# Optimization experiments

Measured on AMD Instinct MI355X. Metric: run time of the kernel, lower is better.

Reference implementation:

```python
import jax, jax.numpy as jnp
from jax import lax
import numpy as np


def gru_last(seq, Wih, Whh, bih, bhh):
    """Run a torch-style GRU over seq [N, T, C] and return only h_T [N, H].

    Gate order matches torch.nn.GRU: (r, z, n);
    n = tanh(W_in x + b_in + r * (W_hn h + b_hn)).
    """
    N = seq.shape[0]
    H = Whh.shape[1]

    def step(h, x_t):
        gi = x_t @ Wih.T + bih          # [N, 3H]
        gh = h @ Whh.T + bhh            # [N, 3H]
        i_r, i_z, i_n = jnp.split(gi, 3, axis=-1)
        h_r, h_z, h_n = jnp.split(gh, 3, axis=-1)
        r = jax.nn.sigmoid(i_r + h_r)
        z = jax.nn.sigmoid(i_z + h_z)
        n = jnp.tanh(i_n + r * h_n)
        h_new = (1.0 - z) * n + z * h
        return h_new, None

    h0 = jnp.zeros((N, H), dtype=seq.dtype)
    hT, _ = lax.scan(step, h0, jnp.swapaxes(seq, 0, 1))  # scan over T
    return hT


def setup_inputs() -> dict:
    key = jax.random.key(0)
    ks = jax.random.split(key, 12)
    B, C, T, Fq, H = 8, 64, 256, 256, 128
    s = 0.05
    return {
        "x": jax.random.normal(ks[0], (B, C, T, Fq), dtype=jnp.float32),
        "Wih_t": jax.random.normal(ks[1], (3 * H, C), dtype=jnp.float32) * s,
        "Whh_t": jax.random.normal(ks[2], (3 * H, H), dtype=jnp.float32) * s,
        "bih_t": jax.random.normal(ks[3], (3 * H,), dtype=jnp.float32) * s,
        "bhh_t": jax.random.normal(ks[4], (3 * H,), dtype=jnp.float32) * s,
        "Wih_f": jax.random.normal(ks[5], (3 * H, C), dtype=jnp.float32) * s,
        "Whh_f": jax.random.normal(ks[6], (3 * H, H), dtype=jnp.float32) * s,
        "bih_f": jax.random.normal(ks[7], (3 * H,), dtype=jnp.float32) * s,
        "bhh_f": jax.random.normal(ks[8], (3 * H,), dtype=jnp.float32) * s,
        "Wp": jax.random.normal(ks[9], (C, H), dtype=jnp.float32) * s,
        "bp": jax.random.normal(ks[10], (C,), dtype=jnp.float32) * s,
    }


def reference(x, Wih_t, Whh_t, bih_t, bhh_t, Wih_f, Whh_f, bih_f, bhh_f, Wp, bp):
    B, C, T, Fq = x.shape
    H = Whh_t.shape[1]

    # time GRU: sequences of length T, one per (batch, freq)
    t_in = jnp.transpose(x, (0, 3, 2, 1)).reshape(B * Fq, T, C)
    h_t = gru_last(t_in, Wih_t, Whh_t, bih_t, bhh_t)          # [B*F, H]
    t_vec = jnp.transpose(h_t.reshape(B, Fq, H), (0, 2, 1))    # [B, H, F]

    # freq GRU: sequences of length F, one per (batch, time)
    f_in = jnp.transpose(x, (0, 2, 3, 1)).reshape(B * T, Fq, C)
    h_f = gru_last(f_in, Wih_f, Whh_f, bih_f, bhh_f)          # [B*T, H]
    f_vec = jnp.transpose(h_f.reshape(B, T, H), (0, 2, 1))    # [B, H, T]

    # t_feat [B,H,F,1] expanded along dim2 to T (requires F == T),
    # f_feat [B,H,T,1] expanded along dim3 to F; fused is constant along F.
    s = t_vec + f_vec                                          # [B, H, T]  (F == T)
    out_t = jnp.einsum("ch,bht->bct", Wp, s) + bp[None, :, None]  # 1x1 conv
    return jnp.broadcast_to(out_t[:, :, :, None], (B, C, T, Fq))
```

## Files before the change

kernel.cpp:

```cpp
#include <hip/hip_runtime.h>

#define B_ 8
#define C_ 64
#define T_ 256
#define F_ 256
#define H_ 128
#define TF_ (T_*F_)

typedef _Float16 half_t;
typedef _Float16 half8 __attribute__((ext_vector_type(8)));
typedef float float4v __attribute__((ext_vector_type(4)));

#if __has_builtin(__builtin_amdgcn_exp2f)
#define EXP2F(x) __builtin_amdgcn_exp2f(x)
#else
static __device__ inline float EXP2F(float x) { float r; asm("v_exp_f32 %0, %1" : "=v"(r) : "v"(x)); return r; }
#endif
#if __has_builtin(__builtin_amdgcn_rcpf)
#define RCPF(x) __builtin_amdgcn_rcpf(x)
#else
static __device__ inline float RCPF(float x) { float r; asm("v_rcp_f32 %0, %1" : "=v"(r) : "v"(x)); return r; }
#endif

#define NEG_L2E  (-1.4426950408889634f)
#define NEG_2L2E (-2.8853900817779268f)

#define XS_M 72
#define XS_S 1160

__device__ inline half8 load_w8s(const float* __restrict__ p, float s) {
    half8 r;
#pragma unroll
    for (int k = 0; k < 8; ++k) r[k] = (half_t)(p[k] * s);
    return r;
}

#define MFMA(a, b, c) __builtin_amdgcn_mfma_f32_16x16x32_f16((a), (b), (c), 0, 0, 0)

__global__ __launch_bounds__(512, 2) void k_gru(
    const float* __restrict__ x,
    const float* __restrict__ Wih_t, const float* __restrict__ Whh_t,
    const float* __restrict__ bih_t, const float* __restrict__ bhh_t,
    const float* __restrict__ Wih_f, const float* __restrict__ Whh_f,
    const float* __restrict__ bih_f, const float* __restrict__ bhh_f,
    float* __restrict__ h_t_out, float* __restrict__ h_f_out) {
    __shared__ half_t hbuf0[16 * 136];
    __shared__ half_t hbuf1[16 * 136];
    __shared__ half_t xt0[8 * XS_S];
    __shared__ half_t xt1[8 * XS_S];

    int tid  = threadIdx.x;
    int w    = tid >> 6;
    int lane = tid & 63;
    int nidx = lane & 15;
    int quad = lane >> 4;

    int bi  = blockIdx.x;
    bool isf = bi >= 128;
    int lbi = bi & 127;
    int b   = lbi >> 4;
    int g16 = (lbi & 15) << 4;

    const float* Wih = isf ? Wih_f : Wih_t;
    const float* Whh = isf ? Whh_f : Whh_t;
    const float* bih = isf ? bih_f : bih_t;
    const float* bhh = isf ? bhh_f : bhh_t;
    float* hout      = isf ? h_f_out : h_t_out;

    int fq, rowid;
    if (!isf) { fq = tid & 3; rowid = tid >> 2; }
    else      { fq = tid & 1; rowid = tid >> 1; }
    int goff[4], ldsoff[4];
#pragma unroll
    for (int j = 0; j < 4; ++j) {
        int row = rowid + (isf ? 256 : 128) * j;
        int c   = isf ? (row >> 4) : (row >> 3);
        int tl  = isf ? (row & 15) : (row & 7);
        goff[j]   = c * 65536 + tl * 256 + 4 * fq;
        ldsoff[j] = isf ? ((4 * fq) * XS_S + tl * XS_M + c)
                        : (tl * XS_S + (4 * fq) * XS_M + c);
    }
    int estr = isf ? XS_S : XS_M;
    int As8  = isf ? 8 : 8 * 256;
    const float* gb = x + (size_t)b * (64 * 65536) + (size_t)(isf ? g16 * 256 : g16);

#define XLOADG()                                                                \
    {                                                                           \
        _Pragma("unroll")                                                       \
        for (int j = 0; j < 4; ++j) rS[j] = *(const float4v*)(gb + goff[j]);    \
        gb += As8;                                                              \
    }
#define XWRITE(XT)                                                              \
    {                                                                           \
        _Pragma("unroll")                                                       \
        for (int j = 0; j < 4; ++j) {                                           \
            _Pragma("unroll")                                                   \
            for (int e = 0; e < 4; ++e)                                         \
                (XT)[ldsoff[j] + e * estr] = (half_t)rS[j][e];                  \
        }                                                                       \
    }

    int gr = w * 16 + nidx;
    int gz = gr + 128;
    int gn = gr + 256;
    int ko = quad * 8;

    half8 wir0 = load_w8s(Wih + gr * 64 + ko,      NEG_L2E);
    half8 wir1 = load_w8s(Wih + gr * 64 + 32 + ko, NEG_L2E);
    half8 wiz0 = load_w8s(Wih + gz * 64 + ko,      NEG_L2E);
    half8 wiz1 = load_w8s(Wih + gz * 64 + 32 + ko, NEG_L2E);
    half8 win0 = load_w8s(Wih + gn * 64 + ko,      NEG_2L2E);
    half8 win1 = load_w8s(Wih + gn * 64 + 32 + ko, NEG_2L2E);
    half8 whr[4], whz[4], whn[4];
#pragma unroll
    for (int kt = 0; kt < 4; ++kt) {
        whr[kt] = load_w8s(Whh + gr * 128 + kt * 32 + ko, NEG_L2E);
        whz[kt] = load_w8s(Whh + gz * 128 + kt * 32 + ko, NEG_L2E);
        whn[kt] = load_w8s(Whh + gn * 128 + kt * 32 + ko, NEG_2L2E);
    }
    float br  = NEG_L2E  * (bih[gr] + bhh[gr]);
    float bz  = NEG_L2E  * (bih[gz] + bhh[gz]);
    float bin = NEG_2L2E * bih[gn];
    float bhn = NEG_2L2E * bhh[gn];
    float4v brv  = {br, br, br, br};
    float4v bzv  = {bz, bz, bz, bz};
    float4v bnv  = {bin, bin, bin, bin};
    float4v bhnv = {bhn, bhn, bhn, bhn};

    for (int idx = tid; idx < 16 * 136; idx += 512) hbuf0[idx] = (half_t)0.f;
    float h_old[4] = {0.f, 0.f, 0.f, 0.f};

    float4v rS[4];
    XLOADG(); XWRITE(xt0);
    XLOADG(); XWRITE(xt1);
    XLOADG();
    __syncthreads();

    float4v xrE, xzE, xnE;
    {
        const half_t* xrp = xt0 + nidx * XS_M + ko;
        half8 a0 = *(const half8*)xrp;
        half8 a1 = *(const half8*)(xrp + 32);
        xrE = MFMA(a0, wir0, brv); xrE = MFMA(a1, wir1, xrE);
        xzE = MFMA(a0, wiz0, bzv); xzE = MFMA(a1, wiz1, xzE);
        xnE = MFMA(a0, win0, bnv); xnE = MFMA(a1, win1, xnE);
    }
    float4v xrO = {0.f, 0.f, 0.f, 0.f};
    float4v xzO = {0.f, 0.f, 0.f, 0.f};
    float4v xnO = {0.f, 0.f, 0.f, 0.f};

#define GRU_STEP(RBUF, WBUF, XR, XZ, XN, XRn, XZn, XNn, XTB, SROW, REF, STG)    \
    {                                                                           \
        const half_t* hrow = (RBUF) + nidx * 136 + ko;                          \
        half8 ha0 = *(const half8*)(hrow);                                      \
        half8 ha1 = *(const half8*)(hrow + 32);                                 \
        half8 ha2 = *(const half8*)(hrow + 64);                                 \
        half8 ha3 = *(const half8*)(hrow + 96);                                 \
        half8 c0x, c1x;                                                         \
        if (REF) {                                                              \
            const half_t* xrp = (XTB) + (SROW) * XS_S + nidx * XS_M + ko;       \
            c0x = *(const half8*)xrp;                                           \
            c1x = *(const half8*)(xrp + 32);                                    \
        }                                                                       \
        XR = MFMA(ha0, whr[0], XR); XR = MFMA(ha1, whr[1], XR);                 \
        XR = MFMA(ha2, whr[2], XR); XR = MFMA(ha3, whr[3], XR);                 \
        XZ = MFMA(ha0, whz[0], XZ); XZ = MFMA(ha1, whz[1], XZ);                 \
        XZ = MFMA(ha2, whz[2], XZ); XZ = MFMA(ha3, whz[3], XZ);                 \
        float4v hnv = MFMA(ha0, whn[0], bhnv);                                  \
        hnv = MFMA(ha1, whn[1], hnv);                                           \
        float rr[4], Ez[4];                                                     \
        _Pragma("unroll")                                                       \
        for (int rg = 0; rg < 4; ++rg) rr[rg] = RCPF(1.f + EXP2F(XR[rg]));      \
        hnv = MFMA(ha2, whn[2], hnv);                                           \
        hnv = MFMA(ha3, whn[3], hnv);                                           \
        _Pragma("unroll")                                                       \
        for (int rg = 0; rg < 4; ++rg) Ez[rg] = EXP2F(XZ[rg]);                  \
        if (REF) {                                                              \
            XRn = MFMA(c0x, wir0, brv); XRn = MFMA(c1x, wir1, XRn);             \
            XZn = MFMA(c0x, wiz0, bzv); XZn = MFMA(c1x, wiz1, XZn);             \
            XNn = MFMA(c0x, win0, bnv); XNn = MFMA(c1x, win1, XNn);             \
        }                                                                       \
        STG                                                                     \
        _Pragma("unroll")                                                       \
        for (int rg = 0; rg < 4; ++rg) {                                        \
            float np  = XN[rg] + rr[rg] * hnv[rg];                              \
            float En  = EXP2F(np);                                              \
            float u   = __builtin_fmaf(h_old[rg], En, h_old[rg]);               \
            float t2  = u + Ez[rg];                                             \
            float num = __builtin_fmaf(-En, Ez[rg], t2);                        \
            float den = (1.f + En) * (1.f + Ez[rg]);                            \
            float h   = num * RCPF(den);                                        \
            h_old[rg] = h;                                                      \
            (WBUF)[(quad * 4 + rg) * 136 + w * 16 + nidx] = (half_t)h;          \
        }                                                                       \
        __syncthreads();                                                        \
    }

    for (int tt = 0; tt < 16; ++tt) {
        GRU_STEP(hbuf0, hbuf1, xrE, xzE, xnE, xrO, xzO, xnO, xt0, 1, 1, {})
        GRU_STEP(hbuf1, hbuf0, xrO, xzO, xnO, xrE, xzE, xnE, xt0, 2, 1, {})
        GRU_STEP(hbuf0, hbuf1, xrE, xzE, xnE, xrO, xzO, xnO, xt0, 3, 1, {})
        GRU_STEP(hbuf1, hbuf0, xrO, xzO, xnO, xrE, xzE, xnE, xt0, 4, 1, {})
        GRU_STEP(hbuf0, hbuf1, xrE, xzE, xnE, xrO, xzO, xnO, xt0, 5, 1, {})
        GRU_STEP(hbuf1, hbuf0, xrO, xzO, xnO, xrE, xzE, xnE, xt0, 6, 1, {})
        GRU_STEP(hbuf0, hbuf1, xrE, xzE, xnE, xrO, xzO, xnO, xt0, 7, 1, {})
        GRU_STEP(hbuf1, hbuf0, xrO, xzO, xnO, xrE, xzE, xnE, xt1, 0, 1,
                 { if (tt < 15) { XWRITE(xt0); XLOADG(); } })
        GRU_STEP(hbuf0, hbuf1, xrE, xzE, xnE, xrO, xzO, xnO, xt1, 1, 1, {})
        GRU_STEP(hbuf1, hbuf0, xrO, xzO, xnO, xrE, xzE, xnE, xt1, 2, 1, {})
        GRU_STEP(hbuf0, hbuf1, xrE, xzE, xnE, xrO, xzO, xnO, xt1, 3, 1, {})
        GRU_STEP(hbuf1, hbuf0, xrO, xzO, xnO, xrE, xzE, xnE, xt1, 4, 1, {})
        GRU_STEP(hbuf0, hbuf1, xrE, xzE, xnE, xrO, xzO, xnO, xt1, 5, 1, {})
        GRU_STEP(hbuf1, hbuf0, xrO, xzO, xnO, xrE, xzE, xnE, xt1, 6, 1, {})
        GRU_STEP(hbuf0, hbuf1, xrE, xzE, xnE, xrO, xzO, xnO, xt1, 7, 1, {})
        GRU_STEP(hbuf1, hbuf0, xrO, xzO, xnO, xrE, xzE, xnE, xt0, 0, (tt < 15),
                 { if (tt < 15) { XWRITE(xt1); if (tt < 14) { XLOADG(); } } })
    }
#undef GRU_STEP
#undef XWRITE
#undef XLOADG

    int srow = (b << 8) + g16;
#pragma unroll
    for (int rg = 0; rg < 4; ++rg) {
        hout[(size_t)(srow + quad * 4 + rg) * H_ + w * 16 + nidx] = h_old[rg];
    }
}

__global__ __launch_bounds__(256) void k_out(const float* __restrict__ h_t,
                                             const float* __restrict__ h_f,
                                             const float* __restrict__ Wp,
                                             const float* __restrict__ bp,
                                             float* __restrict__ out) {
    __shared__ float sv[128];
    __shared__ float part[4][64];
    __shared__ float orow[64];
    int blk = blockIdx.x;
    int b = blk >> 8;
    int i = blk & 255;
    int tid = threadIdx.x;
    size_t hoff = ((size_t)(b * 256 + i)) * 128;
    if (tid < 128) sv[tid] = h_t[hoff + tid] + h_f[hoff + tid];
    __syncthreads();
    int c = tid & 63;
    int q = tid >> 6;
    float p = 0.f;
    const float* wp = Wp + c * 128 + q * 32;
#pragma unroll
    for (int k = 0; k < 32; ++k) p += wp[k] * sv[q * 32 + k];
    part[q][c] = p;
    __syncthreads();
    if (tid < 64) orow[tid] = part[0][tid] + part[1][tid] + part[2][tid] + part[3][tid] + bp[tid];
    __syncthreads();
    int wv   = tid >> 6;
    int lane = tid & 63;
#pragma unroll
    for (int itr = 0; itr < 16; ++itr) {
        int cc = itr * 4 + wv;
        float v = orow[cc];
        float4v vv = {v, v, v, v};
        __builtin_nontemporal_store(vv, (float4v*)(out + (((size_t)(b * 64 + cc)) * 256 + i) * 256 + lane * 4));
    }
}

extern "C" void kernel_launch(void* const* d_in, const int* in_sizes, int n_in,
                              void* d_out, int out_size, void* d_ws, size_t ws_size,
                              hipStream_t stream) {
    const float* x     = (const float*)d_in[0];
    const float* Wih_t = (const float*)d_in[1];
    const float* Whh_t = (const float*)d_in[2];
    const float* bih_t = (const float*)d_in[3];
    const float* bhh_t = (const float*)d_in[4];
    const float* Wih_f = (const float*)d_in[5];
    const float* Whh_f = (const float*)d_in[6];
    const float* bih_f = (const float*)d_in[7];
    const float* bhh_f = (const float*)d_in[8];
    const float* Wp    = (const float*)d_in[9];
    const float* bp    = (const float*)d_in[10];
    float* out = (float*)d_out;

    float* h_t_out = (float*)((char*)d_ws);
    float* h_f_out = (float*)((char*)d_ws + (size_t)2048 * 128 * 4);

    k_gru<<<256, 512, 0, stream>>>(x, Wih_t, Whh_t, bih_t, bhh_t,
                                   Wih_f, Whh_f, bih_f, bhh_f, h_t_out, h_f_out);
    k_out<<<2048, 256, 0, stream>>>(h_t_out, h_f_out, Wp, bp, out);
}
```

Measured before the change: 387.7 us.

## Swizzle LDS layouts for h and x tiles and use a raw barrier

Applies an XOR/rotation-style swizzle to the shared-memory layouts of the hidden-state buffers and the staged input tiles, with matching read offsets precomputed per lane, so the half8 MFMA operand reads and scalar h writes avoid LDS bank conflicts. It also replaces __syncthreads with an inline s_waitcnt lgkmcnt(0) plus s_barrier, which may drop waits on outstanding global loads. The gain would come from fewer LDS conflict stalls on the serial recurrence path. The cost is more complex index arithmetic and some risk of ordering bugs from the weaker barrier.

```diff
diff --git a/kernel.cpp b/kernel.cpp
--- a/kernel.cpp
+++ b/kernel.cpp
@@ -24,6 +24,8 @@
 
 #define NEG_L2E  (-1.4426950408889634f)
 #define NEG_2L2E (-2.8853900817779268f)
+
+#define BAR() asm volatile("s_waitcnt lgkmcnt(0)\n\ts_barrier" ::: "memory")
 
 #define XS_M 72
 #define XS_S 1160
@@ -67,21 +69,46 @@
     const float* bhh = isf ? bhh_f : bhh_t;
     float* hout      = isf ? h_f_out : h_t_out;
 
+    int rrn  = (-2 * nidx) & 7;
+    int xrd0 = nidx * XS_M + (((quad + rrn) & 7) << 3);
+    int xrd1 = nidx * XS_M + (((quad + 4 + rrn) & 7) << 3);
+    int hrd[4];
+#pragma unroll
+    for (int ht = 0; ht < 4; ++ht) {
+        int t = 4 * ht + quad;
+        hrd[ht] = nidx * 136 + (((t & 8) | ((t + rrn) & 7)) << 3);
+    }
+    int hw4[4];
+    {
+        int tch = 2 * w + (nidx >> 3);
+#pragma unroll
+        for (int rg = 0; rg < 4; ++rg) {
+            int rr = (8 - 2 * rg) & 7;
+            hw4[rg] = (quad * 4 + rg) * 136 +
+                      (((tch & 8) | ((tch + rr) & 7)) << 3) + (nidx & 7);
+        }
+    }
+
     int fq, rowid;
     if (!isf) { fq = tid & 3; rowid = tid >> 2; }
     else      { fq = tid & 1; rowid = tid >> 1; }
-    int goff[4], ldsoff[4];
+    int goff[4], ldsoff[4], c3v[4];
 #pragma unroll
     for (int j = 0; j < 4; ++j) {
         int row = rowid + (isf ? 256 : 128) * j;
         int c   = isf ? (row >> 4) : (row >> 3);
         int tl  = isf ? (row & 15) : (row & 7);
-        goff[j]   = c * 65536 + tl * 256 + 4 * fq;
-        ldsoff[j] = isf ? ((4 * fq) * XS_S + tl * XS_M + c)
-                        : (tl * XS_S + (4 * fq) * XS_M + c);
-    }
-    int estr = isf ? XS_S : XS_M;
-    int As8  = isf ? 8 : 8 * 256;
+        goff[j] = c * 65536 + tl * 256 + 4 * fq;
+        if (!isf) {
+            ldsoff[j] = tl * XS_S + (4 * fq) * XS_M + (c & 7);
+            c3v[j]    = c >> 3;
+        } else {
+            ldsoff[j] = (4 * fq) * XS_S + tl * XS_M +
+                        ((((c >> 3) + ((-2 * tl) & 7)) & 7) << 3) + (c & 7);
+            c3v[j]    = 0;
+        }
+    }
+    int As8 = isf ? 8 : 8 * 256;
     const float* gb = x + (size_t)b * (64 * 65536) + (size_t)(isf ? g16 * 256 : g16);
 
 #define XLOADG()                                                                \
@@ -92,11 +119,23 @@
     }
 #define XWRITE(XT)                                                              \
     {                                                                           \
-        _Pragma("unroll")                                                       \
-        for (int j = 0; j < 4; ++j) {                                           \
+        if (!isf) {                                                             \
             _Pragma("unroll")                                                   \
-            for (int e = 0; e < 4; ++e)                                         \
-                (XT)[ldsoff[j] + e * estr] = (half_t)rS[j][e];                  \
+            for (int j = 0; j < 4; ++j) {                                       \
+                _Pragma("unroll")                                               \
+                for (int e = 0; e < 4; ++e) {                                   \
+                    const int rot = (8 - 2 * e) & 7;                            \
+                    (XT)[ldsoff[j] + e * XS_M + (((c3v[j] + rot) & 7) << 3)]    \
+                        = (half_t)rS[j][e];                                     \
+                }                                                               \
+            }                                                                   \
+        } else {                                                                \
+            _Pragma("unroll")                                                   \
+            for (int j = 0; j < 4; ++j) {                                       \
+                _Pragma("unroll")                                               \
+                for (int e = 0; e < 4; ++e)                                     \
+                    (XT)[ldsoff[j] + e * XS_S] = (half_t)rS[j][e];              \
+            }                                                                   \
         }                                                                       \
     }
 
@@ -134,13 +173,12 @@
     XLOADG(); XWRITE(xt0);
     XLOADG(); XWRITE(xt1);
     XLOADG();
-    __syncthreads();
+    BAR();
 
     float4v xrE, xzE, xnE;
     {
-        const half_t* xrp = xt0 + nidx * XS_M + ko;
-        half8 a0 = *(const half8*)xrp;
-        half8 a1 = *(const half8*)(xrp + 32);
+        half8 a0 = *(const half8*)(xt0 + xrd0);
+        half8 a1 = *(const half8*)(xt0 + xrd1);
         xrE = MFMA(a0, wir0, brv); xrE = MFMA(a1, wir1, xrE);
         xzE = MFMA(a0, wiz0, bzv); xzE = MFMA(a1, wiz1, xzE);
         xnE = MFMA(a0, win0, bnv); xnE = MFMA(a1, win1, xnE);
@@ -151,16 +189,15 @@
 
 #define GRU_STEP(RBUF, WBUF, XR, XZ, XN, XRn, XZn, XNn, XTB, SROW, REF, STG)    \
     {                                                                           \
-        const half_t* hrow = (RBUF) + nidx * 136 + ko;                          \
-        half8 ha0 = *(const half8*)(hrow);                                      \
-        half8 ha1 = *(const half8*)(hrow + 32);                                 \
-        half8 ha2 = *(const half8*)(hrow + 64);                                 \
-        half8 ha3 = *(const half8*)(hrow + 96);                                 \
+        half8 ha0 = *(const half8*)((RBUF) + hrd[0]);                           \
+        half8 ha1 = *(const half8*)((RBUF) + hrd[1]);                           \
+        half8 ha2 = *(const half8*)((RBUF) + hrd[2]);                           \
+        half8 ha3 = *(const half8*)((RBUF) + hrd[3]);                           \
         half8 c0x, c1x;                                                         \
         if (REF) {                                                              \
-            const half_t* xrp = (XTB) + (SROW) * XS_S + nidx * XS_M + ko;       \
-            c0x = *(const half8*)xrp;                                           \
-            c1x = *(const half8*)(xrp + 32);                                    \
+            const half_t* xb = (XTB) + (SROW) * XS_S;                           \
+            c0x = *(const half8*)(xb + xrd0);                                   \
+            c1x = *(const half8*)(xb + xrd1);                                   \
         }                                                                       \
         XR = MFMA(ha0, whr[0], XR); XR = MFMA(ha1, whr[1], XR);                 \
         XR = MFMA(ha2, whr[2], XR); XR = MFMA(ha3, whr[3], XR);                 \
@@ -191,9 +228,9 @@
             float den = (1.f + En) * (1.f + Ez[rg]);                            \
             float h   = num * RCPF(den);                                        \
             h_old[rg] = h;                                                      \
-            (WBUF)[(quad * 4 + rg) * 136 + w * 16 + nidx] = (half_t)h;          \
+            (WBUF)[hw4[rg]] = (half_t)h;                                        \
         }                                                                       \
-        __syncthreads();                                                        \
+        BAR();                                                                  \
     }
 
     for (int tt = 0; tt < 16; ++tt) {
```

Result: slower. 396.8 us (+2.3%).
